# Optimization experiments

Measured on AMD Instinct MI355X. Metric: run time of the kernel, lower is better.

## Reference

```python
import jax, jax.numpy as jnp
import numpy as np

BATCH, SEQ, H, N = 8, 4096, 512, 64
DT_MIN, DT_MAX = 1e-3, 1e-1


def setup_inputs() -> dict:
    key = jax.random.key(0)
    k1, k2, k3, k4, k5 = jax.random.split(key, 5)
    n = jnp.arange(N, dtype=jnp.float32)
    # HiPPO-LegS diagonal: A[n,n] = -(n+1) -> log|diag(A)| = log(n+1)
    A_log = jnp.broadcast_to(jnp.log(n + 1.0), (H, N))
    Bv = jnp.broadcast_to(jnp.sqrt(2.0 * n + 1.0), (H, N))
    C = jax.random.normal(k1, (H, N), dtype=jnp.float32) * 0.01
    D = jnp.ones((H,), dtype=jnp.float32)
    log_dt = jax.random.uniform(k2, (H,), dtype=jnp.float32) * (
        np.log(DT_MAX) - np.log(DT_MIN)) + np.log(DT_MIN)
    # reverse-direction params (bidirectional)
    A_log_r = A_log
    B_r = Bv
    C_r = jax.random.normal(k3, (H, N), dtype=jnp.float32) * 0.01
    # out_bi Linear: weight [H, 2H], bias [H]
    W_bi = jax.random.normal(k4, (H, 2 * H), dtype=jnp.float32) / np.sqrt(2.0 * H)
    b_bi = jnp.zeros((H,), dtype=jnp.float32)
    u = jax.random.normal(k5, (BATCH, SEQ, H), dtype=jnp.float32)
    return {"u": u, "A_log": A_log, "Bv": Bv, "C": C, "D": D,
            "log_dt": log_dt, "A_log_r": A_log_r, "B_r": B_r, "C_r": C_r,
            "W_bi": W_bi, "b_bi": b_bi}


def _conv(u, A_log, Bp, Cp, D, log_dt):
    """Diagonal SSM as FFT convolution. u: [B, L, H]."""
    L = u.shape[1]
    dt = jnp.exp(log_dt)                      # [H]
    eA = jnp.exp(A_log)                       # [H, N]
    A_bar = jnp.exp(-dt[:, None] * eA)        # [H, N]
    B_bar = (A_bar - 1.0) / (-eA) * Bp        # [H, N]
    # log-space power kernel: A_bar^k = exp(k * log A_bar)
    logA = jnp.log(jnp.clip(A_bar, 1e-30, None))
    ks = jnp.arange(L, dtype=u.dtype)
    pows = jnp.exp(ks[None, None, :] * logA[:, :, None])   # [H, N, L]
    K = jnp.einsum('dn,dnl->dl', Cp * B_bar, pows)          # [H, L]
    n_fft = 2 * L
    u_f = jnp.fft.rfft(u, n=n_fft, axis=1)                  # [B, L+1, H] complex
    K_f = jnp.fft.rfft(K, n=n_fft, axis=-1)                 # [H, L+1]
    y = jnp.fft.irfft(u_f * K_f.T[None], n=n_fft, axis=1)[:, :L, :]
    return y + u * D


def reference(u, A_log, Bv, C, D, log_dt, A_log_r, B_r, C_r, W_bi, b_bi):
    y = _conv(u, A_log, Bv, C, D, log_dt)
    yr = jnp.flip(_conv(jnp.flip(u, 1), A_log_r, B_r, C_r, D, log_dt), 1)
    ycat = jnp.concatenate([y, yr], axis=-1)                # [B, L, 2H]
    return ycat @ W_bi.T + b_bi
```

## Files before the change

### kernel.cpp

```cpp
#include <hip/hip_runtime.h>
#include <hip/hip_bf16.h>
#include <stdint.h>

#define L_SEQ  4096
#define H_DIM  512
#define N_ST   64
#define N_B    8
#define N_CH   16
#define T_CH   256
#define K_GEMM 1024

typedef float  f32x4  __attribute__((ext_vector_type(4)));
typedef __bf16 bf16x8 __attribute__((ext_vector_type(8)));
typedef __bf16 bf16x4 __attribute__((ext_vector_type(4)));
typedef unsigned short u16x8 __attribute__((ext_vector_type(8)));
typedef unsigned long long ull;

#define GLOAD16(g, l) __builtin_amdgcn_global_load_lds( \
    (const __attribute__((address_space(1))) void*)(g), \
    (__attribute__((address_space(3))) void*)(l), 16, 0, 0)

__global__ __launch_bounds__(256) void k_precompute(
    const float* __restrict__ A_log, const float* __restrict__ Bv,
    const float* __restrict__ C, const float* __restrict__ log_dt,
    const float* __restrict__ A_log_r, const float* __restrict__ B_r,
    const float* __restrict__ C_r,
    float* __restrict__ pA, float* __restrict__ pCB, float* __restrict__ pPW,
    float* __restrict__ pLG)
{
    int tid = blockIdx.x * 256 + threadIdx.x;
    int n   = tid & 63;
    int h   = (tid >> 6) & 511;
    int dir = tid >> 15;
    float dt = expf(log_dt[h]);
    const float* Al = dir ? A_log_r : A_log;
    const float* Bp = dir ? B_r    : Bv;
    const float* Cp = dir ? C_r    : C;
    float eA = expf(Al[h * N_ST + n]);
    float Ab = expf(-dt * eA);
    float Bb = (1.0f - Ab) / eA * Bp[h * N_ST + n];
    pA[tid]  = Ab;
    pCB[tid] = Cp[h * N_ST + n] * Bb;
    pPW[tid] = expf(-dt * eA * (float)T_CH);
    pLG[tid] = -dt * eA * 1.44269504088896f;
}

__global__ __launch_bounds__(256) void k_convw(
    const float* __restrict__ W, __bf16* __restrict__ Wbf)
{
    int tid = blockIdx.x * 256 + threadIdx.x;
    Wbf[tid] = (__bf16)W[tid];
}

__global__ __launch_bounds__(256) void k_kk(
    const float* __restrict__ pCB, const float* __restrict__ pLG,
    float* __restrict__ kk)
{
    __shared__ float scb[64], slg[64];
    int dirh = blockIdx.x;
    int d = threadIdx.x;
    if (d < 64) { scb[d] = pCB[dirh * 64 + d]; slg[d] = pLG[dirh * 64 + d]; }
    __syncthreads();
    float s = 0.f;
    #pragma unroll
    for (int n = 0; n < 64; ++n) s += scb[n] * exp2f((float)d * slg[n]);
    kk[dirh * 256 + d] = s;
}

__global__ __launch_bounds__(256) void k_ut(
    const float* __restrict__ u, __bf16* __restrict__ ut)
{
    __shared__ float tl[32][65];
    int blk = blockIdx.x;
    int lt = blk & 127, ht = (blk >> 7) & 7, b = blk >> 10;
    int t = threadIdx.x;
    int ho = t & 63, li = t >> 6;
    #pragma unroll
    for (int it = 0; it < 8; ++it) {
        int l = it * 4 + li;
        tl[l][ho] = u[(size_t)(b * L_SEQ + lt * 32 + l) * H_DIM + ht * 64 + ho];
    }
    __syncthreads();
    int hh = t >> 2, lrun = (t & 3) * 8;
    bf16x8 v;
    #pragma unroll
    for (int i = 0; i < 8; ++i) v[i] = (__bf16)tl[lrun + i][hh];
    *(bf16x8*)(ut + (size_t)(ht * 64 + hh) * 32768 + b * 4096 + lt * 32 + lrun) = v;
}

__global__ __launch_bounds__(512, 2) void k_state(
    const __bf16* __restrict__ ut, const float* __restrict__ pLG,
    __bf16* __restrict__ S2)
{
    __shared__ __bf16 uts[16384];
    int h = blockIdx.x;
    int t = threadIdx.x;
    int lane = t & 63, w = t >> 6;
    int lr = lane & 15, lg = lane >> 4;
    int dir = w >> 2, mtile = w & 3;

    float s = pLG[(size_t)(dir * 512 + h) * 64 + mtile * 16 + lr];

    bf16x8 Mf[8];
    #pragma unroll
    for (int kk = 0; kk < 8; ++kk) {
        #pragma unroll
        for (int jj = 0; jj < 8; ++jj) {
            int j = kk * 32 + lg * 8 + jj;
            float e = dir ? (float)j : (float)(255 - j);
            Mf[kk][jj] = (__bf16)exp2f(e * s);
        }
    }

    for (int hf = 0; hf < 2; ++hf) {
        if (hf) __syncthreads();
        #pragma unroll
        for (int i = 0; i < 4; ++i) {
            int chunk = i * 512 + t;
            int col   = chunk >> 5;
            int l8    = (chunk & 31) << 3;
            int l8s   = l8 ^ ((col & 7) << 3);
            GLOAD16(ut + (size_t)h * 32768 + (hf * 64 + col) * 256 + l8s,
                    (char*)uts + chunk * 16);
        }
        __syncthreads();

        #pragma unroll
        for (int ntile = 0; ntile < 4; ++ntile) {
            f32x4 acc = {};
            #pragma unroll
            for (int kk = 0; kk < 8; ++kk) {
                int col = ntile * 16 + lr;
                bf16x8 bv = *(const bf16x8*)((char*)uts + col * 512
                             + (((kk * 4 + lg) ^ (col & 7)) << 4));
                acc = __builtin_amdgcn_mfma_f32_16x16x32_bf16(Mf[kk], bv, acc, 0, 0, 0);
            }
            int colg = hf * 64 + ntile * 16 + lr;
            int nq   = mtile * 4 + lg;
            bf16x4 o;
            #pragma unroll
            for (int r = 0; r < 4; ++r) o[r] = (__bf16)acc[r];
            *(bf16x4*)(S2 + ((size_t)((dir * 512 + h) * 16 + nq) * 128 + colg) * 4) = o;
        }
    }
}

__global__ __launch_bounds__(256) void k_chunkscan(
    const float* __restrict__ pPW, __bf16* __restrict__ S2)
{
    int tid = blockIdx.x * 256 + threadIdx.x;
    int b   = tid & 7;
    int nq  = (tid >> 3) & 15;
    int h   = (tid >> 7) & 511;
    int dir = tid >> 16;
    f32x4 pw4 = *(const f32x4*)(pPW + (size_t)(dir * 512 + h) * 64 + nq * 4);
    __bf16* base = S2 + ((size_t)((dir * 512 + h) * 16 + nq) * 128 + b * 16) * 4;
    bf16x8 v[8];
    #pragma unroll
    for (int i = 0; i < 8; ++i) v[i] = *(const bf16x8*)(base + i * 8);
    float X0 = 0.f, X1 = 0.f, X2 = 0.f, X3 = 0.f;
#define SCAN_STEP(c) do { \
    float t0 = (float)v[(c)>>1][((c)&1)*4+0]; v[(c)>>1][((c)&1)*4+0] = (__bf16)X0; X0 = fmaf(pw4[0], X0, t0); \
    float t1 = (float)v[(c)>>1][((c)&1)*4+1]; v[(c)>>1][((c)&1)*4+1] = (__bf16)X1; X1 = fmaf(pw4[1], X1, t1); \
    float t2 = (float)v[(c)>>1][((c)&1)*4+2]; v[(c)>>1][((c)&1)*4+2] = (__bf16)X2; X2 = fmaf(pw4[2], X2, t2); \
    float t3 = (float)v[(c)>>1][((c)&1)*4+3]; v[(c)>>1][((c)&1)*4+3] = (__bf16)X3; X3 = fmaf(pw4[3], X3, t3); \
    } while (0)
    if (dir == 0) {
        #pragma unroll
        for (int c = 0; c < 16; ++c) SCAN_STEP(c);
    } else {
        #pragma unroll
        for (int c = 15; c >= 0; --c) SCAN_STEP(c);
    }
#undef SCAN_STEP
    #pragma unroll
    for (int i = 0; i < 8; ++i) *(bf16x8*)(base + i * 8) = v[i];
}

template<int DIR>
__device__ __forceinline__ void conv_body(
    int h, int t,
    const float* __restrict__ kk, const float* __restrict__ pLG,
    const float* __restrict__ pCB, const float* __restrict__ Dv,
    const __bf16* __restrict__ ut, const __bf16* __restrict__ S,
    __bf16* __restrict__ ycT,
    __bf16* uts, ull* kkq8, float* slg, float* scb)
{
    int dirh = DIR * 512 + h;
    int lane = t & 63, w = t >> 6;
    int lr = lane & 15, lg = lane >> 4;

    unsigned short* asc = (unsigned short*)uts;
    for (int i = t; i < 548; i += 512) {
        int d = DIR ? (i - 272) : (271 - i);
        float kv = (d >= 0 && d < 256) ? kk[dirh * 256 + d] : 0.f;
        asc[i] = __builtin_bit_cast(unsigned short, (__bf16)kv);
    }
    if (t < 64)       slg[t]      = pLG[dirh * 64 + t];
    else if (t < 128) scb[t - 64] = pCB[dirh * 64 + (t - 64)];
    __syncthreads();
    for (int i = t; i < 544; i += 512)
        kkq8[i] = (ull)asc[i] | ((ull)asc[i+1] << 16) | ((ull)asc[i+2] << 32)
                | ((ull)asc[i+3] << 48);
    __syncthreads();

    float Dh = Dv[h];
    const ull* kq = kkq8;

    for (int hf = 0; hf < 2; ++hf) {
        #pragma unroll
        for (int i = 0; i < 4; ++i) {
            int chunk = i * 512 + t;
            int col   = chunk >> 5;
            int l8    = (chunk & 31) << 3;
            int l8s   = l8 ^ ((col & 7) << 3);
            GLOAD16(ut + (size_t)h * 32768 + (hf * 64 + col) * 256 + l8s,
                    (char*)uts + chunk * 16);
        }
        __syncthreads();

        f32x4 acc[2][4] = {};

        #pragma unroll
        for (int mf = 0; mf < 2; ++mf) {
            int rt  = mf ? (15 - w) : w;
            int jlo = DIR ? (rt >> 1) : 0;
            int jhi = DIR ? 8 : ((rt >> 1) + 1);
            int sb  = (DIR ? 272 : 271) + lg * 8 - rt * 16 - lr;
            for (int jt = jlo; jt < jhi; ++jt) {
                bf16x8 bv[4];
                #pragma unroll
                for (int n = 0; n < 4; ++n) {
                    int col = n * 16 + lr;
                    bv[n] = *(const bf16x8*)((char*)uts + col * 512
                              + (((jt * 4 + lg) ^ (col & 7)) << 4));
                }
                int si = sb + jt * 32;
                ull lo = kq[si], hi = kq[si + 4];
                bf16x8 av;
                ((ull*)&av)[0] = lo; ((ull*)&av)[1] = hi;
                #pragma unroll
                for (int n = 0; n < 4; ++n)
                    acc[mf][n] = __builtin_amdgcn_mfma_f32_16x16x32_bf16(av, bv[n], acc[mf][n], 0, 0, 0);
            }
        }

        #pragma unroll
        for (int nt = 0; nt < 2; ++nt) {
            bf16x8 bs[4];
            #pragma unroll
            for (int n = 0; n < 4; ++n) {
                int colg = (hf * 4 + n) * 16 + lr;
                int nq0  = nt * 8 + lg * 2;
                const __bf16* sp = S + ((size_t)((DIR * 512 + h) * 16 + nq0) * 128 + colg) * 4;
                bf16x4 s0 = *(const bf16x4*)(sp);
                bf16x4 s1 = *(const bf16x4*)(sp + 512);
                #pragma unroll
                for (int j = 0; j < 4; ++j) { bs[n][j] = s0[j]; bs[n][4 + j] = s1[j]; }
            }
            #pragma unroll
            for (int mf = 0; mf < 2; ++mf) {
                int rt = mf ? (15 - w) : w;
                int l  = rt * 16 + lr;
                float e = DIR ? (float)(256 - l) : (float)(l + 1);
                bf16x8 gv;
                #pragma unroll
                for (int j = 0; j < 8; ++j) {
                    int n = nt * 32 + lg * 8 + j;
                    gv[j] = (__bf16)(scb[n] * exp2f(e * slg[n]));
                }
                #pragma unroll
                for (int n = 0; n < 4; ++n)
                    acc[mf][n] = __builtin_amdgcn_mfma_f32_16x16x32_bf16(gv, bs[n], acc[mf][n], 0, 0, 0);
            }
        }

        #pragma unroll
        for (int mf = 0; mf < 2; ++mf) {
            int rt = mf ? (15 - w) : w;
            int l0 = rt * 16 + lg * 4;
            #pragma unroll
            for (int n = 0; n < 4; ++n) {
                int col = n * 16 + lr;
                bf16x4 uv = *(const bf16x4*)((char*)uts + col * 512
                             + ((((l0 >> 3) ^ (col & 7)) << 4) | ((l0 & 7) * 2)));
                bf16x4 o;
                #pragma unroll
                for (int r = 0; r < 4; ++r)
                    o[r] = (__bf16)(acc[mf][n][r] + Dh * (float)uv[r]);
                *(bf16x4*)(ycT + (size_t)dirh * 32768 + (hf * 64 + col) * 256 + l0) = o;
            }
        }
        __syncthreads();
    }
}

__global__ __launch_bounds__(512, 4) void k_conv(
    const float* __restrict__ kk, const float* __restrict__ pLG,
    const float* __restrict__ pCB, const float* __restrict__ Dv,
    const __bf16* __restrict__ ut, const __bf16* __restrict__ S,
    __bf16* __restrict__ ycT)
{
    __shared__ __bf16 uts[16384];
    __shared__ ull kkq8[544];
    __shared__ float slg[64], scb[64];
    int h = blockIdx.x & 511;
    int t = threadIdx.x;
    if (blockIdx.x >> 9)
        conv_body<1>(h, t, kk, pLG, pCB, Dv, ut, S, ycT, uts, kkq8, slg, scb);
    else
        conv_body<0>(h, t, kk, pLG, pCB, Dv, ut, S, ycT, uts, kkq8, slg, scb);
}

__global__ __launch_bounds__(256, 2) void k_gemm(
    const __bf16* __restrict__ ycT, const __bf16* __restrict__ B,
    const float* __restrict__ bias, float* __restrict__ out)
{
    __shared__ __bf16 As[2][4][128][8];
    __shared__ __bf16 Bs[2][256][32];
    int t  = threadIdx.x;
    int l  = t & 63, w = t >> 6;
    int lr = l & 15, lg = l >> 4;
    int mBase = blockIdx.y * 128;
    int nBase = blockIdx.x * 256;
    int wr = (w >> 1) * 64, wc = (w & 1) * 128;

    int sT  = t & 15;
    int skk = t >> 4;
    int swz = (sT & 7) << 4;

    f32x4 acc[4][8] = {};
    const __bf16* aptr = ycT + mBase + sT * 8;

#define STAGE_A(buf, va0, va1) do { \
    char* AsB_ = (char*)&As[buf][0][0][0]; \
    _Pragma("unroll") \
    for (int p = 0; p < 2; ++p) { \
        int kk_ = skk + p * 16; \
        u16x8 av_ = p ? (va1) : (va0); \
        int kgrp_ = kk_ >> 3, ke_ = kk_ & 7; \
        _Pragma("unroll") \
        for (int i = 0; i < 8; ++i) { \
            int off_ = ((kgrp_ * 128 + sT * 8 + i) * 16 + ke_ * 2) ^ swz; \
            *(unsigned short*)(AsB_ + off_) = av_[i]; \
        } \
    } } while (0)

#define STAGE_B(buf, kt_) do { \
    char* BsB_ = (char*)&Bs[buf][0][0]; \
    _Pragma("unroll") \
    for (int i = 0; i < 4; ++i) { \
        int chunk_ = i * 256 + t; \
        int row_ = chunk_ >> 2, kq_ = chunk_ & 3; \
        int kqs_ = kq_ ^ ((row_ >> 1) & 3); \
        GLOAD16(B + (size_t)(nBase + row_) * K_GEMM + (kt_) + kqs_ * 8, \
                BsB_ + chunk_ * 16); \
    } } while (0)

#define COMPUTE(buf) do { \
    char* AsB_ = (char*)&As[buf][0][0][0]; \
    char* BsB_ = (char*)&Bs[buf][0][0]; \
    bf16x8 af_[4], bfv_[8]; \
    _Pragma("unroll") \
    for (int m = 0; m < 4; ++m) { \
        int row_ = wr + m * 16 + lr; \
        int off_ = ((lg * 128 + row_) * 16) ^ (((row_ >> 3) & 7) << 4); \
        af_[m] = *(const bf16x8*)(AsB_ + off_); \
    } \
    _Pragma("unroll") \
    for (int n = 0; n < 8; ++n) { \
        int row_ = wc + n * 16 + lr; \
        bfv_[n] = *(const bf16x8*)(BsB_ + row_ * 64 \
                    + ((lg * 16) ^ (((row_ >> 1) & 3) << 4))); \
    } \
    _Pragma("unroll") \
    for (int m = 0; m < 4; ++m) \
        _Pragma("unroll") \
        for (int n = 0; n < 8; ++n) \
            acc[m][n] = __builtin_amdgcn_mfma_f32_16x16x32_bf16(af_[m], bfv_[n], acc[m][n], 0, 0, 0); \
    } while (0)

    u16x8 a0 = *(const u16x8*)(aptr + (size_t)skk * 32768);
    u16x8 a1 = *(const u16x8*)(aptr + (size_t)(skk + 16) * 32768);
    STAGE_A(0, a0, a1);
    STAGE_B(0, 0);
    asm volatile("s_waitcnt vmcnt(0)" ::: "memory");
    __builtin_amdgcn_sched_barrier(0);
    a0 = *(const u16x8*)(aptr + (size_t)(32 + skk) * 32768);
    a1 = *(const u16x8*)(aptr + (size_t)(48 + skk) * 32768);
    __builtin_amdgcn_sched_barrier(0);
    asm volatile("s_waitcnt lgkmcnt(0)" ::: "memory");
    __builtin_amdgcn_s_barrier();

    int cur = 0;
    for (int kt = 0; kt < K_GEMM - 32; kt += 32) {
        int nxt = cur ^ 1;
        STAGE_A(nxt, a0, a1);
        STAGE_B(nxt, kt + 32);
        COMPUTE(cur);
        asm volatile("s_waitcnt vmcnt(0)" ::: "memory");
        __builtin_amdgcn_sched_barrier(0);
        if (kt + 64 < K_GEMM) {
            a0 = *(const u16x8*)(aptr + (size_t)(kt + 64 + skk) * 32768);
            a1 = *(const u16x8*)(aptr + (size_t)(kt + 80 + skk) * 32768);
        }
        __builtin_amdgcn_sched_barrier(0);
        asm volatile("s_waitcnt lgkmcnt(0)" ::: "memory");
        __builtin_amdgcn_s_barrier();
        cur = nxt;
    }
    COMPUTE(cur);

#undef STAGE_A
#undef STAGE_B
#undef COMPUTE

    #pragma unroll
    for (int n = 0; n < 8; ++n) {
        int colg = nBase + wc + n * 16 + lr;
        float bv = bias[colg];
        #pragma unroll
        for (int m = 0; m < 4; ++m) {
            int rowg = mBase + wr + m * 16 + lg * 4;
            #pragma unroll
            for (int r = 0; r < 4; ++r)
                out[(size_t)(rowg + r) * H_DIM + colg] = acc[m][n][r] + bv;
        }
    }
}

extern "C" void kernel_launch(void* const* d_in, const int* in_sizes, int n_in,
                              void* d_out, int out_size, void* d_ws, size_t ws_size,
                              hipStream_t stream)
{
    const float* u       = (const float*)d_in[0];
    const float* A_log   = (const float*)d_in[1];
    const float* Bv      = (const float*)d_in[2];
    const float* C       = (const float*)d_in[3];
    const float* D       = (const float*)d_in[4];
    const float* log_dt  = (const float*)d_in[5];
    const float* A_log_r = (const float*)d_in[6];
    const float* B_r     = (const float*)d_in[7];
    const float* C_r     = (const float*)d_in[8];
    const float* W_bi    = (const float*)d_in[9];
    const float* b_bi    = (const float*)d_in[10];
    float* out = (float*)d_out;

    char* ws = (char*)d_ws;
    float* pA   = (float*)(ws + 0x000000);
    float* pCB  = (float*)(ws + 0x040000);
    float* pPW  = (float*)(ws + 0x080000);
    float* pLG  = (float*)(ws + 0x0C0000);
    float* kk   = (float*)(ws + 0x100000);
    __bf16* Wbf = (__bf16*)(ws + 0x200000);
    __bf16* S   = (__bf16*)(ws + 0x300000);
    __bf16* ut  = (__bf16*)(ws + 0x1300000);
    __bf16* ycT = (__bf16*)(ws + 0x3300000);

    k_precompute<<<256,  256, 0, stream>>>(A_log, Bv, C, log_dt, A_log_r, B_r, C_r,
                                           pA, pCB, pPW, pLG);
    k_convw     <<<2048, 256, 0, stream>>>(W_bi, Wbf);
    k_kk        <<<1024, 256, 0, stream>>>(pCB, pLG, kk);
    k_ut        <<<8192, 256, 0, stream>>>(u, ut);
    k_state     <<<512,  512, 0, stream>>>(ut, pLG, S);
    k_chunkscan <<<512,  256, 0, stream>>>(pPW, S);
    k_conv      <<<1024, 512, 0, stream>>>(kk, pLG, pCB, D, ut, S, ycT);
    dim3 g(2, 256);
    k_gemm      <<<g,    256, 0, stream>>>(ycT, Wbf, b_bi, out);
}
```

Baseline: 147.0 us.

## Fuse precompute into kk, W cast into transpose, chunk scan into state kernel

Folds the parameter precompute into k_kk and the W-to-bf16 cast into the transpose kernel. It replaces the separate chunk-scan kernel with a wave-level shuffle prefix scan done inside k_state on the fp32 MFMA accumulators. It also hoists the decay-matrix fragment generation out of the conv inner loop into registers, and changes the GEMM A staging to pack two k values per 32-bit LDS store. This cuts the launch count from eight to five, removes a global round trip of the state tensor, and removes redundant exp2 work, at the cost of extra registers and shuffle work in k_state and k_conv.

```diff
diff --git a/kernel.cpp b/kernel.cpp
--- a/kernel.cpp
+++ b/kernel.cpp
@@ -20,46 +20,34 @@
     (const __attribute__((address_space(1))) void*)(g), \
     (__attribute__((address_space(3))) void*)(l), 16, 0, 0)
 
-__global__ __launch_bounds__(256) void k_precompute(
+__global__ __launch_bounds__(256) void k_kk(
     const float* __restrict__ A_log, const float* __restrict__ Bv,
     const float* __restrict__ C, const float* __restrict__ log_dt,
     const float* __restrict__ A_log_r, const float* __restrict__ B_r,
     const float* __restrict__ C_r,
-    float* __restrict__ pA, float* __restrict__ pCB, float* __restrict__ pPW,
-    float* __restrict__ pLG)
-{
-    int tid = blockIdx.x * 256 + threadIdx.x;
-    int n   = tid & 63;
-    int h   = (tid >> 6) & 511;
-    int dir = tid >> 15;
-    float dt = expf(log_dt[h]);
-    const float* Al = dir ? A_log_r : A_log;
-    const float* Bp = dir ? B_r    : Bv;
-    const float* Cp = dir ? C_r    : C;
-    float eA = expf(Al[h * N_ST + n]);
-    float Ab = expf(-dt * eA);
-    float Bb = (1.0f - Ab) / eA * Bp[h * N_ST + n];
-    pA[tid]  = Ab;
-    pCB[tid] = Cp[h * N_ST + n] * Bb;
-    pPW[tid] = expf(-dt * eA * (float)T_CH);
-    pLG[tid] = -dt * eA * 1.44269504088896f;
-}
-
-__global__ __launch_bounds__(256) void k_convw(
-    const float* __restrict__ W, __bf16* __restrict__ Wbf)
-{
-    int tid = blockIdx.x * 256 + threadIdx.x;
-    Wbf[tid] = (__bf16)W[tid];
-}
-
-__global__ __launch_bounds__(256) void k_kk(
-    const float* __restrict__ pCB, const float* __restrict__ pLG,
-    float* __restrict__ kk)
+    float* __restrict__ kk, float* __restrict__ pLG,
+    float* __restrict__ pCB, float* __restrict__ pPW)
 {
     __shared__ float scb[64], slg[64];
     int dirh = blockIdx.x;
+    int dir  = dirh >> 9, h = dirh & 511;
     int d = threadIdx.x;
-    if (d < 64) { scb[d] = pCB[dirh * 64 + d]; slg[d] = pLG[dirh * 64 + d]; }
+    if (d < 64) {
+        int n = d;
+        float dt = expf(log_dt[h]);
+        const float* Al = dir ? A_log_r : A_log;
+        const float* Bp = dir ? B_r    : Bv;
+        const float* Cp = dir ? C_r    : C;
+        float eA = expf(Al[h * N_ST + n]);
+        float Ab = expf(-dt * eA);
+        float Bb = (1.0f - Ab) / eA * Bp[h * N_ST + n];
+        float cb = Cp[h * N_ST + n] * Bb;
+        float lg = -dt * eA * 1.44269504088896f;
+        scb[n] = cb; slg[n] = lg;
+        pCB[dirh * 64 + n] = cb;
+        pLG[dirh * 64 + n] = lg;
+        pPW[dirh * 64 + n] = expf(-dt * eA * (float)T_CH);
+    }
     __syncthreads();
     float s = 0.f;
     #pragma unroll
@@ -68,7 +56,8 @@
 }
 
 __global__ __launch_bounds__(256) void k_ut(
-    const float* __restrict__ u, __bf16* __restrict__ ut)
+    const float* __restrict__ u, __bf16* __restrict__ ut,
+    const float* __restrict__ W, __bf16* __restrict__ Wbf)
 {
     __shared__ float tl[32][65];
     int blk = blockIdx.x;
@@ -80,6 +69,10 @@
         int l = it * 4 + li;
         tl[l][ho] = u[(size_t)(b * L_SEQ + lt * 32 + l) * H_DIM + ht * 64 + ho];
     }
+    if (blk < 2048) {
+        int i = blk * 256 + t;
+        Wbf[i] = (__bf16)W[i];
+    }
     __syncthreads();
     int hh = t >> 2, lrun = (t & 3) * 8;
     bf16x8 v;
@@ -90,7 +83,7 @@
 
 __global__ __launch_bounds__(512, 2) void k_state(
     const __bf16* __restrict__ ut, const float* __restrict__ pLG,
-    __bf16* __restrict__ S2)
+    const float* __restrict__ pPW, __bf16* __restrict__ S2)
 {
     __shared__ __bf16 uts[16384];
     int h = blockIdx.x;
@@ -100,6 +93,7 @@
     int dir = w >> 2, mtile = w & 3;
 
     float s = pLG[(size_t)(dir * 512 + h) * 64 + mtile * 16 + lr];
+    f32x4 pw4 = *(const f32x4*)(pPW + (size_t)(dir * 512 + h) * 64 + mtile * 16 + lg * 4);
 
     bf16x8 Mf[8];
     #pragma unroll
@@ -135,46 +129,60 @@
                              + (((kk * 4 + lg) ^ (col & 7)) << 4));
                 acc = __builtin_amdgcn_mfma_f32_16x16x32_bf16(Mf[kk], bv, acc, 0, 0, 0);
             }
+            f32x4 X;
+            if (dir == 0) {
+                f32x4 incl = acc;
+                float p0 = pw4[0], p1 = pw4[1], p2 = pw4[2], p3 = pw4[3];
+                #pragma unroll
+                for (int st = 1; st <= 8; st <<= 1) {
+                    float u0 = __shfl(incl[0], (lane - st) & 63);
+                    float u1 = __shfl(incl[1], (lane - st) & 63);
+                    float u2 = __shfl(incl[2], (lane - st) & 63);
+                    float u3 = __shfl(incl[3], (lane - st) & 63);
+                    if (lr >= st) {
+                        incl[0] = fmaf(p0, u0, incl[0]);
+                        incl[1] = fmaf(p1, u1, incl[1]);
+                        incl[2] = fmaf(p2, u2, incl[2]);
+                        incl[3] = fmaf(p3, u3, incl[3]);
+                    }
+                    p0 *= p0; p1 *= p1; p2 *= p2; p3 *= p3;
+                }
+                #pragma unroll
+                for (int r = 0; r < 4; ++r) {
+                    float sh = __shfl(incl[r], (lane - 1) & 63);
+                    X[r] = (lr == 0) ? 0.f : sh;
+                }
+            } else {
+                f32x4 incl = acc;
+                float p0 = pw4[0], p1 = pw4[1], p2 = pw4[2], p3 = pw4[3];
+                #pragma unroll
+                for (int st = 1; st <= 8; st <<= 1) {
+                    float u0 = __shfl(incl[0], (lane + st) & 63);
+                    float u1 = __shfl(incl[1], (lane + st) & 63);
+                    float u2 = __shfl(incl[2], (lane + st) & 63);
+                    float u3 = __shfl(incl[3], (lane + st) & 63);
+                    if (lr <= 15 - st) {
+                        incl[0] = fmaf(p0, u0, incl[0]);
+                        incl[1] = fmaf(p1, u1, incl[1]);
+                        incl[2] = fmaf(p2, u2, incl[2]);
+                        incl[3] = fmaf(p3, u3, incl[3]);
+                    }
+                    p0 *= p0; p1 *= p1; p2 *= p2; p3 *= p3;
+                }
+                #pragma unroll
+                for (int r = 0; r < 4; ++r) {
+                    float sh = __shfl(incl[r], (lane + 1) & 63);
+                    X[r] = (lr == 15) ? 0.f : sh;
+                }
+            }
             int colg = hf * 64 + ntile * 16 + lr;
             int nq   = mtile * 4 + lg;
             bf16x4 o;
             #pragma unroll
-            for (int r = 0; r < 4; ++r) o[r] = (__bf16)acc[r];
+            for (int r = 0; r < 4; ++r) o[r] = (__bf16)X[r];
             *(bf16x4*)(S2 + ((size_t)((dir * 512 + h) * 16 + nq) * 128 + colg) * 4) = o;
         }
     }
-}
-
-__global__ __launch_bounds__(256) void k_chunkscan(
-    const float* __restrict__ pPW, __bf16* __restrict__ S2)
-{
-    int tid = blockIdx.x * 256 + threadIdx.x;
-    int b   = tid & 7;
-    int nq  = (tid >> 3) & 15;
-    int h   = (tid >> 7) & 511;
-    int dir = tid >> 16;
-    f32x4 pw4 = *(const f32x4*)(pPW + (size_t)(dir * 512 + h) * 64 + nq * 4);
-    __bf16* base = S2 + ((size_t)((dir * 512 + h) * 16 + nq) * 128 + b * 16) * 4;
-    bf16x8 v[8];
-    #pragma unroll
-    for (int i = 0; i < 8; ++i) v[i] = *(const bf16x8*)(base + i * 8);
-    float X0 = 0.f, X1 = 0.f, X2 = 0.f, X3 = 0.f;
-#define SCAN_STEP(c) do { \
-    float t0 = (float)v[(c)>>1][((c)&1)*4+0]; v[(c)>>1][((c)&1)*4+0] = (__bf16)X0; X0 = fmaf(pw4[0], X0, t0); \
-    float t1 = (float)v[(c)>>1][((c)&1)*4+1]; v[(c)>>1][((c)&1)*4+1] = (__bf16)X1; X1 = fmaf(pw4[1], X1, t1); \
-    float t2 = (float)v[(c)>>1][((c)&1)*4+2]; v[(c)>>1][((c)&1)*4+2] = (__bf16)X2; X2 = fmaf(pw4[2], X2, t2); \
-    float t3 = (float)v[(c)>>1][((c)&1)*4+3]; v[(c)>>1][((c)&1)*4+3] = (__bf16)X3; X3 = fmaf(pw4[3], X3, t3); \
-    } while (0)
-    if (dir == 0) {
-        #pragma unroll
-        for (int c = 0; c < 16; ++c) SCAN_STEP(c);
-    } else {
-        #pragma unroll
-        for (int c = 15; c >= 0; --c) SCAN_STEP(c);
-    }
-#undef SCAN_STEP
-    #pragma unroll
-    for (int i = 0; i < 8; ++i) *(bf16x8*)(base + i * 8) = v[i];
 }
 
 template<int DIR>
@@ -203,6 +211,21 @@
         kkq8[i] = (ull)asc[i] | ((ull)asc[i+1] << 16) | ((ull)asc[i+2] << 32)
                 | ((ull)asc[i+3] << 48);
     __syncthreads();
+
+    bf16x8 gvv[2][2];
+    #pragma unroll
+    for (int nt = 0; nt < 2; ++nt)
+        #pragma unroll
+        for (int mf = 0; mf < 2; ++mf) {
+            int rt = mf ? (15 - w) : w;
+            int l  = rt * 16 + lr;
+            float e = DIR ? (float)(256 - l) : (float)(l + 1);
+            #pragma unroll
+            for (int j = 0; j < 8; ++j) {
+                int n = nt * 32 + lg * 8 + j;
+                gvv[nt][mf][j] = (__bf16)(scb[n] * exp2f(e * slg[n]));
+            }
+        }
 
     float Dh = Dv[h];
     const ull* kq = kkq8;
@@ -259,20 +282,10 @@
                 for (int j = 0; j < 4; ++j) { bs[n][j] = s0[j]; bs[n][4 + j] = s1[j]; }
             }
             #pragma unroll
-            for (int mf = 0; mf < 2; ++mf) {
-                int rt = mf ? (15 - w) : w;
-                int l  = rt * 16 + lr;
-                float e = DIR ? (float)(256 - l) : (float)(l + 1);
-                bf16x8 gv;
-                #pragma unroll
-                for (int j = 0; j < 8; ++j) {
-                    int n = nt * 32 + lg * 8 + j;
-                    gv[j] = (__bf16)(scb[n] * exp2f(e * slg[n]));
-                }
+            for (int mf = 0; mf < 2; ++mf)
                 #pragma unroll
                 for (int n = 0; n < 4; ++n)
-                    acc[mf][n] = __builtin_amdgcn_mfma_f32_16x16x32_bf16(gv, bs[n], acc[mf][n], 0, 0, 0);
-            }
+                    acc[mf][n] = __builtin_amdgcn_mfma_f32_16x16x32_bf16(gvv[nt][mf], bs[n], acc[mf][n], 0, 0, 0);
         }
 
         #pragma unroll
@@ -326,8 +339,10 @@
     int wr = (w >> 1) * 64, wc = (w & 1) * 128;
 
     int sT  = t & 15;
-    int skk = t >> 4;
-    int swz = (sT & 7) << 4;
+    int sp  = t >> 4;
+    int swz  = (sT & 7) << 4;
+    int kgrp = sp >> 2;
+    int keb  = (sp & 3) * 4;
 
     f32x4 acc[4][8] = {};
     const __bf16* aptr = ycT + mBase + sT * 8;
@@ -335,15 +350,11 @@
 #define STAGE_A(buf, va0, va1) do { \
     char* AsB_ = (char*)&As[buf][0][0][0]; \
     _Pragma("unroll") \
-    for (int p = 0; p < 2; ++p) { \
-        int kk_ = skk + p * 16; \
-        u16x8 av_ = p ? (va1) : (va0); \
-        int kgrp_ = kk_ >> 3, ke_ = kk_ & 7; \
-        _Pragma("unroll") \
-        for (int i = 0; i < 8; ++i) { \
-            int off_ = ((kgrp_ * 128 + sT * 8 + i) * 16 + ke_ * 2) ^ swz; \
-            *(unsigned short*)(AsB_ + off_) = av_[i]; \
-        } \
+    for (int i = 0; i < 8; ++i) { \
+        unsigned v_ = (unsigned)(unsigned short)(va0)[i] \
+                    | ((unsigned)(unsigned short)(va1)[i] << 16); \
+        int off_ = ((kgrp * 128 + sT * 8 + i) * 16 + keb) ^ swz; \
+        *(unsigned*)(AsB_ + off_) = v_; \
     } } while (0)
 
 #define STAGE_B(buf, kt_) do { \
@@ -380,14 +391,14 @@
             acc[m][n] = __builtin_amdgcn_mfma_f32_16x16x32_bf16(af_[m], bfv_[n], acc[m][n], 0, 0, 0); \
     } while (0)
 
-    u16x8 a0 = *(const u16x8*)(aptr + (size_t)skk * 32768);
-    u16x8 a1 = *(const u16x8*)(aptr + (size_t)(skk + 16) * 32768);
+    u16x8 a0 = *(const u16x8*)(aptr + (size_t)(2 * sp) * 32768);
+    u16x8 a1 = *(const u16x8*)(aptr + (size_t)(2 * sp + 1) * 32768);
     STAGE_A(0, a0, a1);
     STAGE_B(0, 0);
     asm volatile("s_waitcnt vmcnt(0)" ::: "memory");
     __builtin_amdgcn_sched_barrier(0);
-    a0 = *(const u16x8*)(aptr + (size_t)(32 + skk) * 32768);
-    a1 = *(const u16x8*)(aptr + (size_t)(48 + skk) * 32768);
+    a0 = *(const u16x8*)(aptr + (size_t)(32 + 2 * sp) * 32768);
+    a1 = *(const u16x8*)(aptr + (size_t)(32 + 2 * sp + 1) * 32768);
     __builtin_amdgcn_sched_barrier(0);
     asm volatile("s_waitcnt lgkmcnt(0)" ::: "memory");
     __builtin_amdgcn_s_barrier();
@@ -401,8 +412,8 @@
         asm volatile("s_waitcnt vmcnt(0)" ::: "memory");
         __builtin_amdgcn_sched_barrier(0);
         if (kt + 64 < K_GEMM) {
-            a0 = *(const u16x8*)(aptr + (size_t)(kt + 64 + skk) * 32768);
-            a1 = *(const u16x8*)(aptr + (size_t)(kt + 80 + skk) * 32768);
+            a0 = *(const u16x8*)(aptr + (size_t)(kt + 64 + 2 * sp) * 32768);
+            a1 = *(const u16x8*)(aptr + (size_t)(kt + 64 + 2 * sp + 1) * 32768);
         }
         __builtin_amdgcn_sched_barrier(0);
         asm volatile("s_waitcnt lgkmcnt(0)" ::: "memory");
@@ -447,7 +458,6 @@
     float* out = (float*)d_out;
 
     char* ws = (char*)d_ws;
-    float* pA   = (float*)(ws + 0x000000);
     float* pCB  = (float*)(ws + 0x040000);
     float* pPW  = (float*)(ws + 0x080000);
     float* pLG  = (float*)(ws + 0x0C0000);
@@ -457,14 +467,11 @@
     __bf16* ut  = (__bf16*)(ws + 0x1300000);
     __bf16* ycT = (__bf16*)(ws + 0x3300000);
 
-    k_precompute<<<256,  256, 0, stream>>>(A_log, Bv, C, log_dt, A_log_r, B_r, C_r,
-                                           pA, pCB, pPW, pLG);
-    k_convw     <<<2048, 256, 0, stream>>>(W_bi, Wbf);
-    k_kk        <<<1024, 256, 0, stream>>>(pCB, pLG, kk);
-    k_ut        <<<8192, 256, 0, stream>>>(u, ut);
-    k_state     <<<512,  512, 0, stream>>>(ut, pLG, S);
-    k_chunkscan <<<512,  256, 0, stream>>>(pPW, S);
-    k_conv      <<<1024, 512, 0, stream>>>(kk, pLG, pCB, D, ut, S, ycT);
+    k_kk   <<<1024, 256, 0, stream>>>(A_log, Bv, C, log_dt, A_log_r, B_r, C_r,
+                                      kk, pLG, pCB, pPW);
+    k_ut   <<<8192, 256, 0, stream>>>(u, ut, W_bi, Wbf);
+    k_state<<<512,  512, 0, stream>>>(ut, pLG, pPW, S);
+    k_conv <<<1024, 512, 0, stream>>>(kk, pLG, pCB, D, ut, S, ycT);
     dim3 g(2, 256);
-    k_gemm      <<<g,    256, 0, stream>>>(ycT, Wbf, b_bi, out);
-}
+    k_gemm <<<g,    256, 0, stream>>>(ycT, Wbf, b_bi, out);
+}
```

Result: faster. 137.7 us (-6.3%).
